# Performance work log

Measured on AMD Instinct MI355X. Metric: run time of the kernel, lower is better.

Reference implementation:

```python
import jax, jax.numpy as jnp
import numpy as np

# Irreps: in1 = 128x0e + 64x1o + 32x2e, in2 = 16x0e (one-hot-style species attr),
# out = 128x0e + 64x1o + 32x2e.  (mul_in, mul_out, l) per CG path (l x 0e -> l).
PATHS = [(128, 128, 0), (64, 64, 1), (32, 32, 2)]
N_SPECIES = 16
N_NODES = 200_000
DIM_IN = sum(u * (2 * l + 1) for u, _, l in PATHS)   # 480
DIM_OUT = sum(w * (2 * l + 1) for _, w, l in PATHS)  # 480


def setup_inputs() -> dict:
    key = jax.random.key(0)
    k = jax.random.split(key, 5)
    return {
        "x": jax.random.normal(k[0], (N_NODES, DIM_IN), dtype=jnp.float32),
        "operand": jax.random.uniform(k[1], (N_NODES, N_SPECIES), dtype=jnp.float32),
        "w0": jax.random.normal(k[2], (128, N_SPECIES, 128), dtype=jnp.float32),
        "w1": jax.random.normal(k[3], (64, N_SPECIES, 64), dtype=jnp.float32),
        "w2": jax.random.normal(k[4], (32, N_SPECIES, 32), dtype=jnp.float32),
    }


def _path(xl, operand, W, alpha):
    # out[z,w,k] = alpha * sum_{u,v} xl[z,u,k] * operand[z,v] * W[u,v,w]
    # Scan over the small species axis v to avoid a huge [Z,u,w] intermediate.
    Z, u, d = xl.shape
    wm = W.shape[2]

    def step(acc, vin):
        Wv, ov = vin  # Wv: [u, w_out], ov: [Z]
        return acc + ov[:, None, None] * jnp.einsum('zuk,uw->zwk', xl, Wv), None

    init = jnp.zeros((Z, wm, d), dtype=xl.dtype)
    out, _ = jax.lax.scan(step, init, (jnp.moveaxis(W, 1, 0), operand.T))
    return alpha * out


def _fctp(x, operand, weights):
    # e3nn FullyConnectedTensorProduct with in2 = pure 0e scalars:
    # w3j(l, 0, l) = I / sqrt(2l+1); path_weight (component/element norm)
    # = sqrt((2l+1) / (mul_in * n_species))  ->  net alpha = 1/sqrt(mul_in*n_species).
    outs, off = [], 0
    for (u, wm, l), W in zip(PATHS, weights):
        d = 2 * l + 1
        xl = x[:, off:off + u * d].reshape(-1, u, d)  # [Z, mul_in, 2l+1]
        off += u * d
        alpha = jnp.float32(1.0 / float(np.sqrt(u * operand.shape[1])))
        out_l = _path(xl, operand, W, alpha)          # [Z, mul_out, 2l+1]
        outs.append(out_l.reshape(-1, wm * d))
    return jnp.concatenate(outs, axis=-1)             # [Z, 480]


def reference(x, operand, w0, w1, w2):
    return _fctp(x, operand, (w0, w1, w2))
```

## Files before the change

kernel.cpp:

```cpp
#include <hip/hip_runtime.h>
#include <stdint.h>


typedef __attribute__((ext_vector_type(8))) _Float16 f16x8;
typedef __attribute__((ext_vector_type(2))) _Float16 f16x2;
typedef __attribute__((ext_vector_type(4))) float f32x4;

__global__ void prep_wt(const float* __restrict__ w0, const float* __restrict__ w1,
                        const float* __restrict__ w2, unsigned short* __restrict__ wt) {
    int i = blockIdx.x * 256 + threadIdx.x;
    int n, kk, BN, base;
    float v;
    if (i < 262144) {
        base = 0;      n = i >> 11; kk = i & 2047; BN = 128;
        v = w0[kk * 128 + n];
    } else if (i < 327680) {
        int r = i - 262144;
        base = 262144; n = r >> 10; kk = r & 1023; BN = 64;
        v = w1[kk * 64 + n];
    } else {
        int r = i - 327680;
        base = 327680; n = r >> 9;  kk = r & 511;  BN = 32;
        v = w2[kk * 32 + n];
    }
    int t = kk >> 6, c = kk & 63;
    union { _Float16 h; unsigned short s; } u;
    u.h = (_Float16)v;
    wt[base + (t * BN + n) * 64 + (c ^ ((n & 7) * 8))] = u.s;
}

__device__ __forceinline__ void gl_lds16(const void* g, void* l) {
    __builtin_amdgcn_global_load_lds(
        (const __attribute__((address_space(1))) unsigned int*)g,
        (__attribute__((address_space(3))) unsigned int*)l, 16, 0, 0);
}

template<int D, int OFF, int K, int BN, int BM, int WM, int WN>
__device__ __forceinline__ void path_run(int bid, const float* __restrict__ x,
        const float* __restrict__ op, const unsigned short* __restrict__ wt,
        float* __restrict__ out, int Z, float alpha, unsigned short* Bsm)
{
    constexpr int NSTEP = K / 64;
    constexpr int WTM = BM / WM, WTN = BN / WN;
    constexpr int TM = WTM / 16, TN = WTN / 16;
    constexpr int CPW = BN / 32;
    constexpr int TILE = BN * 64;
    constexpr int XW = (D == 1) ? 4 : 2;

    const int tid  = threadIdx.x;
    const int lane = tid & 63, wv = tid >> 6;
    const int q    = lane >> 4, l16 = lane & 15;
    const int qh   = q >> 1;
    const int vh   = (q & 1) * 8;
    const int wm0  = (wv / WN) * WTM, wn0 = (wv % WN) * WTN;
    const int M    = Z * D;
    const long m0  = (long)bid * BM;
    const char* xb = (const char*)x;

    int xoff[TM];
    f16x2 oh[TM][4];
    #pragma unroll
    for (int i = 0; i < TM; ++i) {
        long m = m0 + wm0 + i * 16 + l16;
        if (m >= M) m = M - 1;
        int z = (int)(m / D), kr = (int)(m % D);
        xoff[i] = z * 1920 + (OFF + kr) * 4 + (D > 1 ? qh * D * 4 : 0);
        const float* o = op + (size_t)z * 16 + vh;
        #pragma unroll
        for (int j2 = 0; j2 < 4; ++j2)
            oh[i][j2] = f16x2{(_Float16)o[2 * j2], (_Float16)o[2 * j2 + 1]};
    }

    f32x4 acc[TM][TN];
    #pragma unroll
    for (int i = 0; i < TM; ++i)
        #pragma unroll
        for (int j = 0; j < TN; ++j) acc[i][j] = f32x4{0.f, 0.f, 0.f, 0.f};

    float xr0[TM][XW], xr1[TM][XW];

    auto dmaB = [&](int t, int buf) {
        const unsigned short* src = wt + (size_t)t * TILE;
        unsigned short* dst = Bsm + buf * TILE;
        #pragma unroll
        for (int c = 0; c < CPW; ++c) {
            int off = (wv * CPW + c) * 512 + lane * 8;
            gl_lds16(src + off, dst + off);
        }
    };
    auto xloadA = [&](int t) {
        #pragma unroll
        for (int i = 0; i < TM; ++i) {
            if constexpr (D == 1) {
                f32x4 xv = *(const f32x4*)(xb + xoff[i] + t * 16);
                xr0[i][0] = xv[0]; xr0[i][1] = xv[1]; xr0[i][2] = xv[2]; xr0[i][3] = xv[3];
            } else {
                xr0[i][0] = *(const float*)(xb + xoff[i] + (t * 4    ) * D * 4);
                xr0[i][1] = *(const float*)(xb + xoff[i] + (t * 4 + 2) * D * 4);
            }
        }
    };
    auto xloadB = [&](int t) {
        #pragma unroll
        for (int i = 0; i < TM; ++i) {
            if constexpr (D == 1) {
                f32x4 xv = *(const f32x4*)(xb + xoff[i] + t * 16);
                xr1[i][0] = xv[0]; xr1[i][1] = xv[1]; xr1[i][2] = xv[2]; xr1[i][3] = xv[3];
            } else {
                xr1[i][0] = *(const float*)(xb + xoff[i] + (t * 4    ) * D * 4);
                xr1[i][1] = *(const float*)(xb + xoff[i] + (t * 4 + 2) * D * 4);
            }
        }
    };
    auto computeA = [&](int buf) {
        const unsigned short* bb = Bsm + buf * TILE;
        #pragma unroll
        for (int h = 0; h < 2; ++h) {
            f16x8 bfr[TN];
            #pragma unroll
            for (int j = 0; j < TN; ++j) {
                int n = wn0 + j * 16 + l16;
                bfr[j] = *(const f16x8*)(bb + n * 64 + ((h * 32 + q * 8) ^ ((n & 7) * 8)));
            }
            #pragma unroll
            for (int i = 0; i < TM; ++i) {
                float xs;
                if constexpr (D == 1) xs = qh ? xr0[i][h * 2 + 1] : xr0[i][h * 2];
                else                  xs = xr0[i][h];
                _Float16 xh = (_Float16)xs;
                f16x2 xx{xh, xh};
                unsigned int pk[4];
                #pragma unroll
                for (int j2 = 0; j2 < 4; ++j2)
                    pk[j2] = __builtin_bit_cast(unsigned int, xx * oh[i][j2]);
                f16x8 af = __builtin_bit_cast(f16x8, uint4{pk[0], pk[1], pk[2], pk[3]});
                #pragma unroll
                for (int j = 0; j < TN; ++j)
                    acc[i][j] = __builtin_amdgcn_mfma_f32_16x16x32_f16(
                        af, bfr[j], acc[i][j], 0, 0, 0);
            }
        }
    };
    auto computeB = [&](int buf) {
        const unsigned short* bb = Bsm + buf * TILE;
        #pragma unroll
        for (int h = 0; h < 2; ++h) {
            f16x8 bfr[TN];
            #pragma unroll
            for (int j = 0; j < TN; ++j) {
                int n = wn0 + j * 16 + l16;
                bfr[j] = *(const f16x8*)(bb + n * 64 + ((h * 32 + q * 8) ^ ((n & 7) * 8)));
            }
            #pragma unroll
            for (int i = 0; i < TM; ++i) {
                float xs;
                if constexpr (D == 1) xs = qh ? xr1[i][h * 2 + 1] : xr1[i][h * 2];
                else                  xs = xr1[i][h];
                _Float16 xh = (_Float16)xs;
                f16x2 xx{xh, xh};
                unsigned int pk[4];
                #pragma unroll
                for (int j2 = 0; j2 < 4; ++j2)
                    pk[j2] = __builtin_bit_cast(unsigned int, xx * oh[i][j2]);
                f16x8 af = __builtin_bit_cast(f16x8, uint4{pk[0], pk[1], pk[2], pk[3]});
                #pragma unroll
                for (int j = 0; j < TN; ++j)
                    acc[i][j] = __builtin_amdgcn_mfma_f32_16x16x32_f16(
                        af, bfr[j], acc[i][j], 0, 0, 0);
            }
        }
    };

    dmaB(0, 0);
    xloadA(0);
    __syncthreads();

    for (int t = 0; t < NSTEP; t += 2) {
        dmaB(t + 1, 1);
        xloadB(t + 1);
        computeA(0);
        __syncthreads();
        if (t + 2 < NSTEP) { dmaB(t + 2, 0); xloadA(t + 2); }
        computeB(1);
        __syncthreads();
    }

    #pragma unroll
    for (int i = 0; i < TM; ++i) {
        #pragma unroll
        for (int p = 0; p < 4; ++p) {
            long m = m0 + wm0 + i * 16 + q * 4 + p;
            if (m < M) {
                int z = (int)(m / D), k = (int)(m % D);
                float* orow = out + (size_t)z * 480 + OFF + k;
                #pragma unroll
                for (int j = 0; j < TN; ++j) {
                    int col = wn0 + j * 16 + l16;
                    orow[(size_t)col * D] = alpha * acc[i][j][p];
                }
            }
        }
    }
}

__global__ __launch_bounds__(256, 3)
void fctp_fused(const float* __restrict__ x, const float* __restrict__ op,
                const unsigned short* __restrict__ wt, float* __restrict__ out,
                int Z, int nb0, int nb01) {
    __shared__ unsigned short Bsm[2 * 8192];
    int bid = blockIdx.x;
    if (bid < nb0)
        path_run<1, 0, 2048, 128, 128, 2, 2>(bid, x, op, wt, out, Z,
                                             0.02209708691f, Bsm);
    else if (bid < nb01)
        path_run<3, 128, 1024, 64, 256, 4, 1>(bid - nb0, x, op, wt + 262144, out, Z,
                                              0.03125f, Bsm);
    else
        path_run<5, 320, 512, 32, 256, 4, 1>(bid - nb01, x, op, wt + 327680, out, Z,
                                             0.04419417382f, Bsm);
}

extern "C" void kernel_launch(void* const* d_in, const int* in_sizes, int n_in,
                              void* d_out, int out_size, void* d_ws, size_t ws_size,
                              hipStream_t stream) {
    (void)n_in; (void)out_size; (void)ws_size;
    const float* x  = (const float*)d_in[0];
    const float* op = (const float*)d_in[1];
    const float* w0 = (const float*)d_in[2];
    const float* w1 = (const float*)d_in[3];
    const float* w2 = (const float*)d_in[4];
    float* out = (float*)d_out;
    const int Z = in_sizes[0] / 480;

    unsigned short* wt = (unsigned short*)d_ws;
    prep_wt<<<1344, 256, 0, stream>>>(w0, w1, w2, wt);

    const int nb0 = (Z + 127) / 128;
    const int nb1 = (3 * Z + 255) / 256;
    const int nb2 = (5 * Z + 255) / 256;
    fctp_fused<<<nb0 + nb1 + nb2, 256, 0, stream>>>(x, op, wt, out, Z, nb0, nb0 + nb1);
}
```

Baseline: 869.0 us.

## Switch to persistent blocks holding the full weight slice resident in LDS

```diff
diff --git a/kernel.cpp b/kernel.cpp
--- a/kernel.cpp
+++ b/kernel.cpp
@@ -9,24 +9,29 @@
 __global__ void prep_wt(const float* __restrict__ w0, const float* __restrict__ w1,
                         const float* __restrict__ w2, unsigned short* __restrict__ wt) {
     int i = blockIdx.x * 256 + threadIdx.x;
-    int n, kk, BN, base;
-    float v;
+    int idx; float v;
     if (i < 262144) {
-        base = 0;      n = i >> 11; kk = i & 2047; BN = 128;
+        int n = i >> 11, kk = i & 2047;
+        int slice = n >> 5, nn = n & 31;
+        int t = kk >> 6, c = kk & 63;
         v = w0[kk * 128 + n];
+        idx = slice * 65536 + t * 2048 + nn * 64 + (c ^ ((nn & 7) * 8));
     } else if (i < 327680) {
         int r = i - 262144;
-        base = 262144; n = r >> 10; kk = r & 1023; BN = 64;
+        int n = r >> 10, kk = r & 1023;
+        int t = kk >> 6, c = kk & 63;
         v = w1[kk * 64 + n];
+        idx = 262144 + t * 4096 + n * 64 + (c ^ ((n & 7) * 8));
     } else {
         int r = i - 327680;
-        base = 327680; n = r >> 9;  kk = r & 511;  BN = 32;
+        int n = r >> 9, kk = r & 511;
+        int t = kk >> 6, c = kk & 63;
         v = w2[kk * 32 + n];
-    }
-    int t = kk >> 6, c = kk & 63;
+        idx = 327680 + t * 2048 + n * 64 + (c ^ ((n & 7) * 8));
+    }
     union { _Float16 h; unsigned short s; } u;
     u.h = (_Float16)v;
-    wt[base + (t * BN + n) * 64 + (c ^ ((n & 7) * 8))] = u.s;
+    wt[idx] = u.s;
 }
 
 __device__ __forceinline__ void gl_lds16(const void* g, void* l) {
@@ -35,189 +40,213 @@
         (__attribute__((address_space(3))) unsigned int*)l, 16, 0, 0);
 }
 
-template<int D, int OFF, int K, int BN, int BM, int WM, int WN>
-__device__ __forceinline__ void path_run(int bid, const float* __restrict__ x,
-        const float* __restrict__ op, const unsigned short* __restrict__ wt,
-        float* __restrict__ out, int Z, float alpha, unsigned short* Bsm)
+template<int D, int OFF, int K, int BCOL, int WM, int WN>
+__device__ __forceinline__ void path_persist(int zb, int NZB, int colbase,
+        const float* __restrict__ x, const float* __restrict__ op,
+        const unsigned short* __restrict__ wt, float* __restrict__ out,
+        int Z, float alpha, unsigned short* Bsm)
 {
-    constexpr int NSTEP = K / 64;
-    constexpr int WTM = BM / WM, WTN = BN / WN;
-    constexpr int TM = WTM / 16, TN = WTN / 16;
-    constexpr int CPW = BN / 32;
-    constexpr int TILE = BN * 64;
-    constexpr int XW = (D == 1) ? 4 : 2;
+    constexpr int KT  = K / 64;
+    constexpr int NG  = KT / 2;
+    constexpr int TM  = 4;
+    constexpr int TN  = BCOL / (WN * 16);
+    constexpr int CH  = WM * 64;
+    constexpr int TSH = K * BCOL;
+    constexpr int NIT = TSH / (512 * 8);
+    constexpr int XW  = (D == 1) ? 4 : 2;
+    constexpr int TILE = BCOL * 64;
 
     const int tid  = threadIdx.x;
     const int lane = tid & 63, wv = tid >> 6;
     const int q    = lane >> 4, l16 = lane & 15;
     const int qh   = q >> 1;
     const int vh   = (q & 1) * 8;
-    const int wm0  = (wv / WN) * WTM, wn0 = (wv % WN) * WTN;
+    const int wm0  = (wv / WN) * 64;
+    const int wn0  = (wv % WN) * 32;
     const int M    = Z * D;
-    const long m0  = (long)bid * BM;
     const char* xb = (const char*)x;
 
-    int xoff[TM];
-    f16x2 oh[TM][4];
     #pragma unroll
-    for (int i = 0; i < TM; ++i) {
-        long m = m0 + wm0 + i * 16 + l16;
-        if (m >= M) m = M - 1;
-        int z = (int)(m / D), kr = (int)(m % D);
-        xoff[i] = z * 1920 + (OFF + kr) * 4 + (D > 1 ? qh * D * 4 : 0);
-        const float* o = op + (size_t)z * 16 + vh;
-        #pragma unroll
-        for (int j2 = 0; j2 < 4; ++j2)
-            oh[i][j2] = f16x2{(_Float16)o[2 * j2], (_Float16)o[2 * j2 + 1]};
-    }
-
-    f32x4 acc[TM][TN];
-    #pragma unroll
-    for (int i = 0; i < TM; ++i)
-        #pragma unroll
-        for (int j = 0; j < TN; ++j) acc[i][j] = f32x4{0.f, 0.f, 0.f, 0.f};
-
-    float xr0[TM][XW], xr1[TM][XW];
-
-    auto dmaB = [&](int t, int buf) {
-        const unsigned short* src = wt + (size_t)t * TILE;
-        unsigned short* dst = Bsm + buf * TILE;
-        #pragma unroll
-        for (int c = 0; c < CPW; ++c) {
-            int off = (wv * CPW + c) * 512 + lane * 8;
-            gl_lds16(src + off, dst + off);
-        }
-    };
-    auto xloadA = [&](int t) {
+    for (int it = 0; it < NIT; ++it) {
+        int off = it * 4096 + tid * 8;
+        gl_lds16(wt + off, Bsm + off);
+    }
+    __syncthreads();
+
+    const int nch = (M + CH - 1) / CH;
+    const int c0 = (int)((long)zb * nch / NZB);
+    const int c1 = (int)((long)(zb + 1) * nch / NZB);
+
+    for (int c = c0; c < c1; ++c) {
+        const long base = (long)c * CH;
+
+        int xoff[TM];
+        f16x2 oh[TM][4];
         #pragma unroll
         for (int i = 0; i < TM; ++i) {
-            if constexpr (D == 1) {
-                f32x4 xv = *(const f32x4*)(xb + xoff[i] + t * 16);
-                xr0[i][0] = xv[0]; xr0[i][1] = xv[1]; xr0[i][2] = xv[2]; xr0[i][3] = xv[3];
-            } else {
-                xr0[i][0] = *(const float*)(xb + xoff[i] + (t * 4    ) * D * 4);
-                xr0[i][1] = *(const float*)(xb + xoff[i] + (t * 4 + 2) * D * 4);
-            }
+            long m = base + wm0 + i * 16 + l16;
+            if (m >= M) m = M - 1;
+            int z = (int)(m / D), kr = (int)(m % D);
+            xoff[i] = z * 1920 + (OFF + kr) * 4 + (D > 1 ? qh * D * 4 : 0);
+            const f32x4* o4 = (const f32x4*)(op + (size_t)z * 16 + vh);
+            f32x4 oa = o4[0], ob = o4[1];
+            oh[i][0] = f16x2{(_Float16)oa[0], (_Float16)oa[1]};
+            oh[i][1] = f16x2{(_Float16)oa[2], (_Float16)oa[3]};
+            oh[i][2] = f16x2{(_Float16)ob[0], (_Float16)ob[1]};
+            oh[i][3] = f16x2{(_Float16)ob[2], (_Float16)ob[3]};
         }
-    };
-    auto xloadB = [&](int t) {
+
+        f32x4 acc[TM][TN];
+        #pragma unroll
+        for (int i = 0; i < TM; ++i)
+            #pragma unroll
+            for (int j = 0; j < TN; ++j) acc[i][j] = f32x4{0.f, 0.f, 0.f, 0.f};
+
+        float xr0[2][TM][XW], xr1[2][TM][XW];
+
+        auto xloadA = [&](int g) {
+            #pragma unroll
+            for (int tt = 0; tt < 2; ++tt) {
+                int t = g * 2 + tt;
+                #pragma unroll
+                for (int i = 0; i < TM; ++i) {
+                    if constexpr (D == 1) {
+                        f32x4 xv = *(const f32x4*)(xb + xoff[i] + t * 16);
+                        xr0[tt][i][0] = xv[0]; xr0[tt][i][1] = xv[1];
+                        xr0[tt][i][2] = xv[2]; xr0[tt][i][3] = xv[3];
+                    } else {
+                        xr0[tt][i][0] = *(const float*)(xb + xoff[i] + (t * 4    ) * D * 4);
+                        xr0[tt][i][1] = *(const float*)(xb + xoff[i] + (t * 4 + 2) * D * 4);
+                    }
+                }
+            }
+        };
+        auto xloadB = [&](int g) {
+            #pragma unroll
+            for (int tt = 0; tt < 2; ++tt) {
+                int t = g * 2 + tt;
+                #pragma unroll
+                for (int i = 0; i < TM; ++i) {
+                    if constexpr (D == 1) {
+                        f32x4 xv = *(const f32x4*)(xb + xoff[i] + t * 16);
+                        xr1[tt][i][0] = xv[0]; xr1[tt][i][1] = xv[1];
+                        xr1[tt][i][2] = xv[2]; xr1[tt][i][3] = xv[3];
+                    } else {
+                        xr1[tt][i][0] = *(const float*)(xb + xoff[i] + (t * 4    ) * D * 4);
+                        xr1[tt][i][1] = *(const float*)(xb + xoff[i] + (t * 4 + 2) * D * 4);
+                    }
+                }
+            }
+        };
+        auto computeA = [&](int g) {
+            #pragma unroll
+            for (int tt = 0; tt < 2; ++tt) {
+                const unsigned short* tb = Bsm + (g * 2 + tt) * TILE;
+                #pragma unroll
+                for (int h = 0; h < 2; ++h) {
+                    f16x8 bfr[TN];
+                    #pragma unroll
+                    for (int j = 0; j < TN; ++j) {
+                        int n = wn0 + j * 16 + l16;
+                        bfr[j] = *(const f16x8*)(tb + n * 64 + ((h * 32 + q * 8) ^ ((n & 7) * 8)));
+                    }
+                    #pragma unroll
+                    for (int i = 0; i < TM; ++i) {
+                        float xs;
+                        if constexpr (D == 1) xs = qh ? xr0[tt][i][h * 2 + 1] : xr0[tt][i][h * 2];
+                        else                  xs = xr0[tt][i][h];
+                        _Float16 xh = (_Float16)xs;
+                        f16x2 xx{xh, xh};
+                        unsigned int pk[4];
+                        #pragma unroll
+                        for (int j2 = 0; j2 < 4; ++j2)
+                            pk[j2] = __builtin_bit_cast(unsigned int, xx * oh[i][j2]);
+                        f16x8 af = __builtin_bit_cast(f16x8, uint4{pk[0], pk[1], pk[2], pk[3]});
+                        #pragma unroll
+                        for (int j = 0; j < TN; ++j)
+                            acc[i][j] = __builtin_amdgcn_mfma_f32_16x16x32_f16(
+                                af, bfr[j], acc[i][j], 0, 0, 0);
+                    }
+                }
+            }
+        };
+        auto computeB = [&](int g) {
+            #pragma unroll
+            for (int tt = 0; tt < 2; ++tt) {
+                const unsigned short* tb = Bsm + (g * 2 + tt) * TILE;
+                #pragma unroll
+                for (int h = 0; h < 2; ++h) {
+                    f16x8 bfr[TN];
+                    #pragma unroll
+                    for (int j = 0; j < TN; ++j) {
+                        int n = wn0 + j * 16 + l16;
+                        bfr[j] = *(const f16x8*)(tb + n * 64 + ((h * 32 + q * 8) ^ ((n & 7) * 8)));
+                    }
+                    #pragma unroll
+                    for (int i = 0; i < TM; ++i) {
+                        float xs;
+                        if constexpr (D == 1) xs = qh ? xr1[tt][i][h * 2 + 1] : xr1[tt][i][h * 2];
+                        else                  xs = xr1[tt][i][h];
+                        _Float16 xh = (_Float16)xs;
+                        f16x2 xx{xh, xh};
+                        unsigned int pk[4];
+                        #pragma unroll
+                        for (int j2 = 0; j2 < 4; ++j2)
+                            pk[j2] = __builtin_bit_cast(unsigned int, xx * oh[i][j2]);
+                        f16x8 af = __builtin_bit_cast(f16x8, uint4{pk[0], pk[1], pk[2], pk[3]});
+                        #pragma unroll
+                        for (int j = 0; j < TN; ++j)
+                            acc[i][j] = __builtin_amdgcn_mfma_f32_16x16x32_f16(
+                                af, bfr[j], acc[i][j], 0, 0, 0);
+                    }
+                }
+            }
+        };
+
+        xloadA(0);
+        for (int g = 0; g < NG; g += 2) {
+            xloadB(g + 1);
+            computeA(g);
+            if (g + 2 < NG) xloadA(g + 2);
+            computeB(g + 1);
+        }
+
         #pragma unroll
         for (int i = 0; i < TM; ++i) {
-            if constexpr (D == 1) {
-                f32x4 xv = *(const f32x4*)(xb + xoff[i] + t * 16);
-                xr1[i][0] = xv[0]; xr1[i][1] = xv[1]; xr1[i][2] = xv[2]; xr1[i][3] = xv[3];
-            } else {
-                xr1[i][0] = *(const float*)(xb + xoff[i] + (t * 4    ) * D * 4);
-                xr1[i][1] = *(const float*)(xb + xoff[i] + (t * 4 + 2) * D * 4);
+            #pragma unroll
+            for (int p = 0; p < 4; ++p) {
+                long m = base + wm0 + i * 16 + q * 4 + p;
+                if (m < M) {
+                    int z = (int)(m / D), k = (int)(m % D);
+                    float* orow = out + (size_t)z * 480 + OFF + k;
+                    #pragma unroll
+                    for (int j = 0; j < TN; ++j) {
+                        int col = colbase + wn0 + j * 16 + l16;
+                        orow[(size_t)col * D] = alpha * acc[i][j][p];
+                    }
+                }
             }
         }
-    };
-    auto computeA = [&](int buf) {
-        const unsigned short* bb = Bsm + buf * TILE;
-        #pragma unroll
-        for (int h = 0; h < 2; ++h) {
-            f16x8 bfr[TN];
-            #pragma unroll
-            for (int j = 0; j < TN; ++j) {
-                int n = wn0 + j * 16 + l16;
-                bfr[j] = *(const f16x8*)(bb + n * 64 + ((h * 32 + q * 8) ^ ((n & 7) * 8)));
-            }
-            #pragma unroll
-            for (int i = 0; i < TM; ++i) {
-                float xs;
-                if constexpr (D == 1) xs = qh ? xr0[i][h * 2 + 1] : xr0[i][h * 2];
-                else                  xs = xr0[i][h];
-                _Float16 xh = (_Float16)xs;
-                f16x2 xx{xh, xh};
-                unsigned int pk[4];
-                #pragma unroll
-                for (int j2 = 0; j2 < 4; ++j2)
-                    pk[j2] = __builtin_bit_cast(unsigned int, xx * oh[i][j2]);
-                f16x8 af = __builtin_bit_cast(f16x8, uint4{pk[0], pk[1], pk[2], pk[3]});
-                #pragma unroll
-                for (int j = 0; j < TN; ++j)
-                    acc[i][j] = __builtin_amdgcn_mfma_f32_16x16x32_f16(
-                        af, bfr[j], acc[i][j], 0, 0, 0);
-            }
-        }
-    };
-    auto computeB = [&](int buf) {
-        const unsigned short* bb = Bsm + buf * TILE;
-        #pragma unroll
-        for (int h = 0; h < 2; ++h) {
-            f16x8 bfr[TN];
-            #pragma unroll
-            for (int j = 0; j < TN; ++j) {
-                int n = wn0 + j * 16 + l16;
-                bfr[j] = *(const f16x8*)(bb + n * 64 + ((h * 32 + q * 8) ^ ((n & 7) * 8)));
-            }
-            #pragma unroll
-            for (int i = 0; i < TM; ++i) {
-                float xs;
-                if constexpr (D == 1) xs = qh ? xr1[i][h * 2 + 1] : xr1[i][h * 2];
-                else                  xs = xr1[i][h];
-                _Float16 xh = (_Float16)xs;
-                f16x2 xx{xh, xh};
-                unsigned int pk[4];
-                #pragma unroll
-                for (int j2 = 0; j2 < 4; ++j2)
-                    pk[j2] = __builtin_bit_cast(unsigned int, xx * oh[i][j2]);
-                f16x8 af = __builtin_bit_cast(f16x8, uint4{pk[0], pk[1], pk[2], pk[3]});
-                #pragma unroll
-                for (int j = 0; j < TN; ++j)
-                    acc[i][j] = __builtin_amdgcn_mfma_f32_16x16x32_f16(
-                        af, bfr[j], acc[i][j], 0, 0, 0);
-            }
-        }
-    };
-
-    dmaB(0, 0);
-    xloadA(0);
-    __syncthreads();
-
-    for (int t = 0; t < NSTEP; t += 2) {
-        dmaB(t + 1, 1);
-        xloadB(t + 1);
-        computeA(0);
-        __syncthreads();
-        if (t + 2 < NSTEP) { dmaB(t + 2, 0); xloadA(t + 2); }
-        computeB(1);
-        __syncthreads();
-    }
-
-    #pragma unroll
-    for (int i = 0; i < TM; ++i) {
-        #pragma unroll
-        for (int p = 0; p < 4; ++p) {
-            long m = m0 + wm0 + i * 16 + q * 4 + p;
-            if (m < M) {
-                int z = (int)(m / D), k = (int)(m % D);
-                float* orow = out + (size_t)z * 480 + OFF + k;
-                #pragma unroll
-                for (int j = 0; j < TN; ++j) {
-                    int col = wn0 + j * 16 + l16;
-                    orow[(size_t)col * D] = alpha * acc[i][j][p];
-                }
-            }
-        }
-    }
-}
-
-__global__ __launch_bounds__(256, 3)
-void fctp_fused(const float* __restrict__ x, const float* __restrict__ op,
-                const unsigned short* __restrict__ wt, float* __restrict__ out,
-                int Z, int nb0, int nb01) {
-    __shared__ unsigned short Bsm[2 * 8192];
+    }
+}
+
+__global__ __launch_bounds__(512, 1)
+void fctp_persist(const float* __restrict__ x, const float* __restrict__ op,
+                  const unsigned short* __restrict__ wt, float* __restrict__ out,
+                  int Z, int nb0, int nb01, int nbtot) {
+    __shared__ unsigned short Bsm[65536];
     int bid = blockIdx.x;
-    if (bid < nb0)
-        path_run<1, 0, 2048, 128, 128, 2, 2>(bid, x, op, wt, out, Z,
-                                             0.02209708691f, Bsm);
-    else if (bid < nb01)
-        path_run<3, 128, 1024, 64, 256, 4, 1>(bid - nb0, x, op, wt + 262144, out, Z,
-                                              0.03125f, Bsm);
-    else
-        path_run<5, 320, 512, 32, 256, 4, 1>(bid - nb01, x, op, wt + 327680, out, Z,
-                                             0.04419417382f, Bsm);
+    if (bid < nb0) {
+        int zb = bid >> 2, slice = bid & 3;
+        path_persist<1, 0, 2048, 32, 8, 1>(zb, nb0 >> 2, slice * 32, x, op,
+                wt + slice * 65536, out, Z, 0.02209708691f, Bsm);
+    } else if (bid < nb01) {
+        path_persist<3, 128, 1024, 64, 4, 2>(bid - nb0, nb01 - nb0, 0, x, op,
+                wt + 262144, out, Z, 0.03125f, Bsm);
+    } else {
+        path_persist<5, 320, 512, 32, 8, 1>(bid - nb01, nbtot - nb01, 0, x, op,
+                wt + 327680, out, Z, 0.04419417382f, Bsm);
+    }
 }
 
 extern "C" void kernel_launch(void* const* d_in, const int* in_sizes, int n_in,
@@ -235,8 +264,8 @@
     unsigned short* wt = (unsigned short*)d_ws;
     prep_wt<<<1344, 256, 0, stream>>>(w0, w1, w2, wt);
 
-    const int nb0 = (Z + 127) / 128;
-    const int nb1 = (3 * Z + 255) / 256;
-    const int nb2 = (5 * Z + 255) / 256;
-    fctp_fused<<<nb0 + nb1 + nb2, 256, 0, stream>>>(x, op, wt, out, Z, nb0, nb0 + nb1);
-}
+    const int nb0   = 448;
+    const int nb01  = nb0 + 384;
+    const int nbtot = nb01 + 192;
+    fctp_persist<<<nbtot, 512, 0, stream>>>(x, op, wt, out, Z, nb0, nb01, nbtot);
+}
```

Result: slower. 1.312 ms (+50.9%).
